# Kernel tuning notes

Measured on AMD Instinct MI355X. Metric: run time of the kernel, lower is better.

## Reference

```python
import jax, jax.numpy as jnp
import numpy as np

B, N, DIN, DH = 16, 512, 128, 256
NEG = -9.0e15  # matches -9000000000000000.0 in torch source


def _xavier(key, fan_in, fan_out):
    lim = float(np.sqrt(6.0 / (fan_in + fan_out)))
    return jax.random.uniform(key, (fan_in, fan_out), jnp.float32, -lim, lim)


def _l2n(x, eps=1e-12):
    # torch F.normalize: x / max(||x||, eps)
    return x / jnp.maximum(jnp.linalg.norm(x, axis=-1, keepdims=True), eps)


def _prelu(x, a):
    return jnp.where(x >= 0, x, a * x)


def setup_inputs() -> dict:
    key = jax.random.key(0)
    ks = jax.random.split(key, 12)
    seq = jax.random.normal(ks[0], (B, N, DIN), jnp.float32)
    # sparse-ish nonnegative adjacency with self loops, row-normalized
    u = jax.random.uniform(ks[1], (B, N, N), jnp.float32)
    a = jnp.where(u < 0.1, u, 0.0) + jnp.eye(N, dtype=jnp.float32)[None]
    adj = a / a.sum(-1, keepdims=True)
    # dense diffusion matrix, row-normalized
    d = jax.random.uniform(ks[2], (B, N, N), jnp.float32)
    diff = d / d.sum(-1, keepdims=True)
    # dropout keep-mask for F.dropout(p=0.1, training=True)
    keep = jax.random.bernoulli(ks[3], 0.9, (B, N, N)).astype(jnp.float32)
    drop_mask = keep / 0.9
    return {
        "seq": seq, "adj": adj, "diff": diff, "drop_mask": drop_mask,
        "fc1_w": _xavier(ks[4], DIN, DH),
        "q_w": _xavier(ks[5], DH, DH),
        "k_w": _xavier(ks[6], DH, DH),
        "v_w1": _xavier(ks[7], DH, DH),
        "v_w2": _xavier(ks[8], DH, DH),
        "fc2_w": _xavier(ks[9], DIN, DH),
        "bias1": jnp.zeros((DH,), jnp.float32),
        "bias2": jnp.zeros((DH,), jnp.float32),
        "prelu1_a": jnp.float32(0.25),
        "prelu2_a": jnp.float32(0.25),
        "v_prelu_a": jnp.float32(0.25),
    }


def reference(seq, adj, diff, drop_mask, fc1_w, q_w, k_w, v_w1, v_w2,
              fc2_w, bias1, bias2, prelu1_a, prelu2_a, v_prelu_a):
    # ---- GCN1 (attention branch) ----
    fts = seq @ fc1_w                                   # [B,N,H]
    out = jnp.einsum('bmn,bnh->bmh', adj, fts)          # adj aggregation
    q = _l2n(out @ q_w)
    k = _l2n(out @ k_w)
    scores = jax.lax.stop_gradient(jnp.einsum('bmd,bnd->bmn', q, k))  # .detach()
    div_loss = jnp.mean(jnp.sum((q - k) ** 2, axis=-1))
    att = jnp.where(adj > 0, scores, NEG)
    att = jax.nn.softmax(att, axis=-1) * drop_mask      # dropout(p=0.1)
    agg = jnp.einsum('bmn,bnh->bmh', att, out)
    v = _prelu(agg @ v_w1, v_prelu_a) @ v_w2 + bias1
    h1 = _prelu(v, prelu1_a)
    # ---- GCN2 (plain branch) ----
    h2 = _prelu(jnp.einsum('bmn,bnh->bmh', diff, seq @ fc2_w) + bias2, prelu2_a)
    # ---- Readout ----
    c1 = jnp.mean(h1, axis=1)                           # [B,H]
    c2 = jnp.mean(h2, axis=1)
    # ---- DIS ----
    n1 = _l2n(h1).reshape(B * N, DH)
    n2 = _l2n(h2).reshape(B * N, DH)
    node_logits = n1 @ n2.T                             # [B*N, B*N]
    graph_logits = _l2n(c1) @ _l2n(c2).T                # [B, B]
    return node_logits, graph_logits, div_loss
```

## Files before the change

### kernel.cpp

```cpp
#include <hip/hip_runtime.h>
#include <hip/hip_bf16.h>


using bf16x8 = __attribute__((ext_vector_type(8))) short;
using f32x4  = __attribute__((ext_vector_type(4))) float;

__device__ __forceinline__ unsigned short f2b(float f) {
    union { float f; unsigned int u; } x; x.f = f;
    unsigned int r = x.u + 0x7FFFu + ((x.u >> 16) & 1u);
    return (unsigned short)(r >> 16);
}
__device__ __forceinline__ void gload_lds16(const void* g, void* l) {
    __builtin_amdgcn_global_load_lds(
        (const __attribute__((address_space(1))) void*)g,
        (__attribute__((address_space(3))) void*)l, 16, 0, 0);
}

__global__ __launch_bounds__(256) void prep(
    const float* __restrict__ seq, const float* __restrict__ adj,
    const float* __restrict__ diff,
    const float* __restrict__ fc1, const float* __restrict__ fc2,
    const float* __restrict__ qw,  const float* __restrict__ kw,
    const float* __restrict__ v1,  const float* __restrict__ v2,
    unsigned short* __restrict__ seq_bf, unsigned short* __restrict__ adj_bf,
    unsigned short* __restrict__ diff_bf,
    unsigned short* fc1T, unsigned short* fc2T, unsigned short* qwT,
    unsigned short* kwT,  unsigned short* v1T,  unsigned short* v2T)
{
    __shared__ float t[32][33];
    const int bid = blockIdx.x, tid = threadIdx.x;
    if (bid < 9216) {
        long i = (long)bid * 256 + tid;
        const float* src; unsigned short* dst; long off;
        if (i < 262144)       { src = seq;  dst = seq_bf;  off = i; }
        else if (i < 1310720) { src = adj;  dst = adj_bf;  off = i - 262144; }
        else                  { src = diff; dst = diff_bf; off = i - 1310720; }
        float4 v = reinterpret_cast<const float4*>(src)[off];
        ushort4 o; o.x = f2b(v.x); o.y = f2b(v.y); o.z = f2b(v.z); o.w = f2b(v.w);
        reinterpret_cast<ushort4*>(dst)[off] = o;
        return;
    }
    const int r = bid - 9216;
    const int z = r >> 6;
    const float* in; unsigned short* op; int R;
    if      (z == 0) { in = fc1; op = fc1T; R = 128; }
    else if (z == 1) { in = fc2; op = fc2T; R = 128; }
    else if (z == 2) { in = qw;  op = qwT;  R = 256; }
    else if (z == 3) { in = kw;  op = kwT;  R = 256; }
    else if (z == 4) { in = v1;  op = v1T;  R = 256; }
    else             { in = v2;  op = v2T;  R = 256; }
    const int c0 = (r & 7) * 32, r0 = ((r >> 3) & 7) * 32;
    if (r0 >= R) return;
    const int x = tid & 31, y = tid >> 5;
    for (int i = 0; i < 32; i += 8) t[y + i][x] = in[(long)(r0 + y + i) * 256 + c0 + x];
    __syncthreads();
    for (int i = 0; i < 32; i += 8)
        op[(long)(c0 + y + i) * R + r0 + x] = f2b(t[x][y + i]);
}

#define BN 128
#define BK 64

template<int TBM, bool WF, bool WB, bool SWZ>
__global__ __launch_bounds__(256) void gemm_nt(
    const unsigned short* __restrict__ A, const unsigned short* __restrict__ Bt,
    float* __restrict__ Cf, unsigned short* __restrict__ Cb,
    int M, int Nn, int K, int lda, int ldb, int ldc,
    long sA, long sB, long sC)
{
    constexpr int MI = TBM / 32;
    __shared__ unsigned char smem_g[(TBM + BN) * BK * 2];
    unsigned short* As = (unsigned short*)smem_g;
    unsigned short* Bs = (unsigned short*)(smem_g + TBM * BK * 2);
    const int b = blockIdx.z;
    A  += (long)b * sA;
    Bt += (long)b * sB;
    const long cbase = (long)b * sC;

    int tx, ty;
    if (SWZ) {
        int bid = blockIdx.y * gridDim.x + blockIdx.x;
        int nwg = gridDim.x * gridDim.y;
        int cpx = nwg >> 3;
        int s = (bid & 7) * cpx + (bid >> 3);
        tx = s % gridDim.x; ty = s / gridDim.x;
    } else { tx = blockIdx.x; ty = blockIdx.y; }
    const int tile_m = ty * TBM;
    const int tile_n = tx * BN;

    const int tid  = threadIdx.x;
    const int lane = tid & 63;
    const int wave = tid >> 6;
    const int wm = (wave >> 1) * (TBM / 2);
    const int wn = (wave & 1) << 6;
    const int lrow = lane >> 3;
    const int lcol = (lane & 7) << 3;

    f32x4 acc[MI][4] = {};

    for (int k0 = 0; k0 < K; k0 += BK) {
        #pragma unroll
        for (int i = 0; i < TBM / 32; ++i) {
            const int rb = (i * 4 + wave) * 8;
            gload_lds16(A + (long)(tile_m + rb + lrow) * lda + k0 + lcol, &As[rb * BK]);
        }
        #pragma unroll
        for (int i = 0; i < 4; ++i) {
            const int rb = (i * 4 + wave) * 8;
            gload_lds16(Bt + (long)(tile_n + rb + lrow) * ldb + k0 + lcol, &Bs[rb * BK]);
        }
        __syncthreads();
        #pragma unroll
        for (int ks = 0; ks < 2; ++ks) {
            const int kk = ks * 32 + ((lane >> 4) << 3);
            bf16x8 af[MI], bq[4];
            #pragma unroll
            for (int mi = 0; mi < MI; ++mi)
                af[mi] = *reinterpret_cast<const bf16x8*>(&As[(wm + (lane & 15) + mi * 16) * BK + kk]);
            #pragma unroll
            for (int ni = 0; ni < 4; ++ni)
                bq[ni] = *reinterpret_cast<const bf16x8*>(&Bs[(wn + (lane & 15) + ni * 16) * BK + kk]);
            #pragma unroll
            for (int mi = 0; mi < MI; ++mi)
                #pragma unroll
                for (int ni = 0; ni < 4; ++ni)
                    acc[mi][ni] = __builtin_amdgcn_mfma_f32_16x16x32_bf16(
                        af[mi], bq[ni], acc[mi][ni], 0, 0, 0);
        }
        __syncthreads();
    }

    const int c0 = lane & 15;
    const int r0 = (lane >> 4) << 2;

    if (WB) {
        #pragma unroll
        for (int ni = 0; ni < 4; ++ni) {
            const int col = tile_n + wn + ni * 16 + c0;
            #pragma unroll
            for (int mi = 0; mi < MI; ++mi) {
                const int row0 = tile_m + wm + mi * 16 + r0;
                #pragma unroll
                for (int j = 0; j < 4; ++j)
                    Cb[cbase + (long)(row0 + j) * ldc + col] = f2b(acc[mi][ni][j]);
            }
        }
    }
    if (WF) {
        float* bounce = (float*)smem_g;
        const int tr = tid >> 5;
        const int tc = (tid & 31) << 2;
        #pragma unroll
        for (int h = 0; h < 2; ++h) {
            __syncthreads();
            if ((wave >> 1) == h) {
                #pragma unroll
                for (int mi = 0; mi < MI; ++mi)
                    #pragma unroll
                    for (int ni = 0; ni < 4; ++ni)
                        #pragma unroll
                        for (int j = 0; j < 4; ++j)
                            bounce[(mi * 16 + r0 + j) * 128 + wn + ni * 16 + c0] =
                                acc[mi][ni][j];
            }
            __syncthreads();
            #pragma unroll
            for (int p = 0; p < 8; ++p) {
                const int rl = p * 8 + tr;
                f32x4 v = *reinterpret_cast<const f32x4*>(&bounce[rl * 128 + tc]);
                __builtin_nontemporal_store(v, reinterpret_cast<f32x4*>(
                    &Cf[cbase + (long)(tile_m + h * 64 + rl) * ldc + tile_n + tc]));
            }
        }
    }
}

__global__ __launch_bounds__(256) void gcn1qk(
    const unsigned short* __restrict__ adj_bf,
    const unsigned short* __restrict__ ftsT,
    const unsigned short* __restrict__ qkT,
    unsigned short* __restrict__ outT,
    unsigned short* __restrict__ q_bf,
    unsigned short* __restrict__ k_bf)
{
    __shared__ unsigned char smem[73984];
    unsigned short* Ot  = (unsigned short*)smem;
    unsigned short* As  = (unsigned short*)(smem + 8448);
    unsigned short* Bs  = (unsigned short*)(smem + 10496);
    unsigned short* Bs2 = (unsigned short*)(smem + 8448);
    __shared__ float sred[16][4];

    const int b  = blockIdx.y;
    const int m0 = blockIdx.x << 4;
    const unsigned short* ap = adj_bf + ((long)b * 512 + m0) * 512;

    const int tid = threadIdx.x, lane = tid & 63, wave = tid >> 6;
    const int lrow = lane >> 3, lcol = (lane & 7) << 3;
    const int hi = lane >> 4, c0 = lane & 15, r0 = hi << 2;

    {
        const int wn = wave << 6;
        f32x4 acc[4] = {};
        for (int k0 = 0; k0 < 512; k0 += 64) {
            if (wave < 2)
                gload_lds16(ap + (long)(wave * 8 + lrow) * 512 + k0 + lcol, &As[wave * 8 * 64]);
            #pragma unroll
            for (int i = 0; i < 8; ++i) {
                const int rb = (i * 4 + wave) * 8;
                gload_lds16(ftsT + (long)(rb + lrow) * 8192 + b * 512 + k0 + lcol, &Bs[rb * 64]);
            }
            __syncthreads();
            #pragma unroll
            for (int ks = 0; ks < 2; ++ks) {
                const int kk = ks * 32 + (hi << 3);
                bf16x8 af = *reinterpret_cast<const bf16x8*>(&As[c0 * 64 + kk]);
                #pragma unroll
                for (int ni = 0; ni < 4; ++ni) {
                    bf16x8 bq = *reinterpret_cast<const bf16x8*>(&Bs[(wn + ni * 16 + c0) * 64 + kk]);
                    acc[ni] = __builtin_amdgcn_mfma_f32_16x16x32_bf16(af, bq, acc[ni], 0, 0, 0);
                }
            }
            __syncthreads();
        }
        #pragma unroll
        for (int ni = 0; ni < 4; ++ni) {
            const int col = wn + ni * 16 + c0;
            ushort4 o;
            unsigned short* e = (unsigned short*)&o;
            #pragma unroll
            for (int j = 0; j < 4; ++j) {
                unsigned short v = f2b(acc[ni][j]);
                e[j] = v;
                Ot[(r0 + j) * 264 + col] = v;
            }
            *reinterpret_cast<ushort4*>(
                &outT[(long)b * 131072 + (long)col * 512 + m0 + r0]) = o;
        }
    }

    {
        const int wn = wave << 7;
        f32x4 acc[8] = {};
        for (int k0 = 0; k0 < 256; k0 += 64) {
            #pragma unroll
            for (int i = 0; i < 16; ++i) {
                const int rb = (i * 4 + wave) * 8;
                gload_lds16(qkT + (long)(rb + lrow) * 256 + k0 + lcol, &Bs2[rb * 64]);
            }
            __syncthreads();
            #pragma unroll
            for (int ks = 0; ks < 2; ++ks) {
                const int kk = ks * 32 + (hi << 3);
                bf16x8 af = *reinterpret_cast<const bf16x8*>(&Ot[c0 * 264 + k0 + kk]);
                #pragma unroll
                for (int ni = 0; ni < 8; ++ni) {
                    bf16x8 bq = *reinterpret_cast<const bf16x8*>(&Bs2[(wn + ni * 16 + c0) * 64 + kk]);
                    acc[ni] = __builtin_amdgcn_mfma_f32_16x16x32_bf16(af, bq, acc[ni], 0, 0, 0);
                }
            }
            __syncthreads();
        }
        float rs[4] = {};
        #pragma unroll
        for (int ni = 0; ni < 8; ++ni)
            #pragma unroll
            for (int j = 0; j < 4; ++j) { float x = acc[ni][j]; rs[j] += x * x; }
        #pragma unroll
        for (int o = 1; o <= 8; o <<= 1)
            #pragma unroll
            for (int j = 0; j < 4; ++j) rs[j] += __shfl_xor(rs[j], o);
        if (c0 == 0) {
            #pragma unroll
            for (int j = 0; j < 4; ++j) sred[r0 + j][wave] = rs[j];
        }
        __syncthreads();
        float inv[4];
        #pragma unroll
        for (int j = 0; j < 4; ++j) {
            const int rr = r0 + j;
            float sq = sred[rr][0] + sred[rr][1];
            float sk = sred[rr][2] + sred[rr][3];
            inv[j] = 1.f / fmaxf(sqrtf(wave < 2 ? sq : sk), 1e-12f);
        }
        #pragma unroll
        for (int ni = 0; ni < 8; ++ni)
            #pragma unroll
            for (int j = 0; j < 4; ++j) {
                const long rowg = (long)b * 512 + m0 + r0 + j;
                const int col = wn + ni * 16 + c0;
                unsigned short v = f2b(acc[ni][j] * inv[j]);
                if (wave < 2) q_bf[rowg * 256 + col] = v;
                else          k_bf[rowg * 256 + col - 256] = v;
            }
    }
}

__global__ __launch_bounds__(256) void attmlp_h2(
    const unsigned short* __restrict__ q_bf,
    const unsigned short* __restrict__ k_bf,
    const unsigned short* __restrict__ adj_bf,
    const float* __restrict__ drop,
    const unsigned short* __restrict__ outT,
    const unsigned short* __restrict__ w1T,
    const unsigned short* __restrict__ w2T,
    const float* __restrict__ bias1,
    const float* __restrict__ av, const float* __restrict__ a1,
    unsigned short* __restrict__ n1,
    float* __restrict__ psum1,
    float* __restrict__ rowpart,
    const unsigned short* __restrict__ diff_bf,
    const unsigned short* __restrict__ fts2T,
    const float* __restrict__ bias2, const float* __restrict__ a2,
    unsigned short* __restrict__ n2,
    float* __restrict__ psum2)
{
    __shared__ unsigned char smem[69632];
    __shared__ float redm[32][4], reds[32][4];

    const int idx = blockIdx.x >> 1;
    const int tid = threadIdx.x, lane = tid & 63, wave = tid >> 6;
    const int lrow = lane >> 3, lcol = (lane & 7) << 3;
    const int hi = lane >> 4, c0 = lane & 15, r0 = hi << 2;

    if (blockIdx.x & 1) {
        unsigned short* As  = (unsigned short*)smem;
        unsigned short* Bs  = (unsigned short*)(smem + 4096);
        unsigned short* Pls = (unsigned short*)smem;
        unsigned short* Bs2 = (unsigned short*)(smem + 34816);
        unsigned short* T   = (unsigned short*)smem;
        unsigned short* Bs3 = (unsigned short*)(smem + 16896);

        const int b  = idx >> 4;
        const int m0 = (idx & 15) << 5;
        const unsigned short* qp = q_bf + (long)b * 131072 + (long)m0 * 256;
        const unsigned short* kp = k_bf + (long)b * 131072;
        const unsigned short* ot = outT + (long)b * 131072;
        const unsigned short* ap = adj_bf + ((long)b * 512 + m0) * 512;
        const float*          dp = drop   + ((long)b * 512 + m0) * 512;

        {
            const int wn = wave << 7;
            f32x4 acc[2][8] = {};
            for (int k0 = 0; k0 < 256; k0 += 64) {
                gload_lds16(qp + (long)(wave * 8 + lrow) * 256 + k0 + lcol, &As[wave * 8 * 64]);
                #pragma unroll
                for (int i = 0; i < 16; ++i) {
                    const int rb = (i * 4 + wave) * 8;
                    gload_lds16(kp + (long)(rb + lrow) * 256 + k0 + lcol, &Bs[rb * 64]);
                }
                __syncthreads();
                #pragma unroll
                for (int ks = 0; ks < 2; ++ks) {
                    const int kk = ks * 32 + (hi << 3);
                    bf16x8 af[2], bq[8];
                    #pragma unroll
                    for (int mi = 0; mi < 2; ++mi)
                        af[mi] = *reinterpret_cast<const bf16x8*>(&As[(mi * 16 + c0) * 64 + kk]);
                    #pragma unroll
                    for (int ni = 0; ni < 8; ++ni)
                        bq[ni] = *reinterpret_cast<const bf16x8*>(&Bs[(wn + ni * 16 + c0) * 64 + kk]);
                    #pragma unroll
                    for (int mi = 0; mi < 2; ++mi)
                        #pragma unroll
                        for (int ni = 0; ni < 8; ++ni)
                            acc[mi][ni] = __builtin_amdgcn_mfma_f32_16x16x32_bf16(
                                af[mi], bq[ni], acc[mi][ni], 0, 0, 0);
                }
                __syncthreads();
            }

            float rmax[2][4];
            #pragma unroll
            for (int mi = 0; mi < 2; ++mi)
                #pragma unroll
                for (int j = 0; j < 4; ++j) rmax[mi][j] = -3.0e38f;
            #pragma unroll
            for (int mi = 0; mi < 2; ++mi)
                #pragma unroll
                for (int ni = 0; ni < 8; ++ni)
                    #pragma unroll
                    for (int j = 0; j < 4; ++j) {
                        const int rowl = mi * 16 + r0 + j;
                        const int col  = wn + ni * 16 + c0;
                        float s = acc[mi][ni][j];
                        if (col == m0 + rowl)
                            rowpart[(long)b * 512 + m0 + rowl] = 2.f - 2.f * s;
                        bool m = ap[(long)rowl * 512 + col] != 0;
                        s = m ? s : -3.0e38f;
                        acc[mi][ni][j] = s;
                        rmax[mi][j] = fmaxf(rmax[mi][j], s);
                    }
            #pragma unroll
            for (int o = 1; o <= 8; o <<= 1)
                #pragma unroll
                for (int mi = 0; mi < 2; ++mi)
                    #pragma unroll
                    for (int j = 0; j < 4; ++j)
                        rmax[mi][j] = fmaxf(rmax[mi][j], __shfl_xor(rmax[mi][j], o));
            if (c0 == 0) {
                #pragma unroll
                for (int mi = 0; mi < 2; ++mi)
                    #pragma unroll
                    for (int j = 0; j < 4; ++j) redm[mi * 16 + r0 + j][wave] = rmax[mi][j];
            }
            __syncthreads();
            float mx[2][4], rsum[2][4];
            #pragma unroll
            for (int mi = 0; mi < 2; ++mi)
                #pragma unroll
                for (int j = 0; j < 4; ++j) {
                    const int rr = mi * 16 + r0 + j;
                    mx[mi][j] = fmaxf(fmaxf(redm[rr][0], redm[rr][1]),
                                      fmaxf(redm[rr][2], redm[rr][3]));
                    rsum[mi][j] = 0.f;
                }
            #pragma unroll
            for (int mi = 0; mi < 2; ++mi)
                #pragma unroll
                for (int ni = 0; ni < 8; ++ni)
                    #pragma unroll
                    for (int j = 0; j < 4; ++j) {
                        float e = __expf(acc[mi][ni][j] - mx[mi][j]);
                        acc[mi][ni][j] = e;
                        rsum[mi][j] += e;
                    }
            #pragma unroll
            for (int o = 1; o <= 8; o <<= 1)
                #pragma unroll
                for (int mi = 0; mi < 2; ++mi)
                    #pragma unroll
                    for (int j = 0; j < 4; ++j) rsum[mi][j] += __shfl_xor(rsum[mi][j], o);
            if (c0 == 0) {
                #pragma unroll
                for (int mi = 0; mi < 2; ++mi)
                    #pragma unroll
                    for (int j = 0; j < 4; ++j) reds[mi * 16 + r0 + j][wave] = rsum[mi][j];
            }
            __syncthreads();
            float inv[2][4];
            #pragma unroll
            for (int mi = 0; mi < 2; ++mi)
                #pragma unroll
                for (int j = 0; j < 4; ++j) {
                    const int rr = mi * 16 + r0 + j;
                    inv[mi][j] = 1.f / (reds[rr][0] + reds[rr][1] + reds[rr][2] + reds[rr][3]);
                }
            #pragma unroll
            for (int mi = 0; mi < 2; ++mi)
                #pragma unroll
                for (int ni = 0; ni < 8; ++ni)
                    #pragma unroll
                    for (int j = 0; j < 4; ++j) {
                        const int rowl = mi * 16 + r0 + j;
                        const int col  = wn + ni * 16 + c0;
                        float p = acc[mi][ni][j] * inv[mi][j] * dp[(long)rowl * 512 + col];
                        Pls[rowl * 520 + col] = f2b(p);
                    }
        }
        __syncthreads();

        f32x4 acc2[2][4] = {};
        {
            const int wn = wave << 6;
            for (int k0 = 0; k0 < 512; k0 += 64) {
                #pragma unroll
                for (int i = 0; i < 8; ++i) {
                    const int rb = (i * 4 + wave) * 8;
                    gload_lds16(ot + (long)(rb + lrow) * 512 + k0 + lcol, &Bs2[rb * 64]);
                }
                __syncthreads();
                #pragma unroll
                for (int ks = 0; ks < 2; ++ks) {
                    const int kk = ks * 32 + (hi << 3);
                    bf16x8 af[2], bq[4];
                    #pragma unroll
                    for (int mi = 0; mi < 2; ++mi)
                        af[mi] = *reinterpret_cast<const bf16x8*>(&Pls[(mi * 16 + c0) * 520 + k0 + kk]);
                    #pragma unroll
                    for (int ni = 0; ni < 4; ++ni)
                        bq[ni] = *reinterpret_cast<const bf16x8*>(&Bs2[(wn + ni * 16 + c0) * 64 + kk]);
                    #pragma unroll
                    for (int mi = 0; mi < 2; ++mi)
                        #pragma unroll
                        for (int ni = 0; ni < 4; ++ni)
                            acc2[mi][ni] = __builtin_amdgcn_mfma_f32_16x16x32_bf16(
                                af[mi], bq[ni], acc2[mi][ni], 0, 0, 0);
                }
                __syncthreads();
            }
        }

        const int wn6 = wave << 6;
        const float alphav = av[0];
        #pragma unroll
        for (int mi = 0; mi < 2; ++mi)
            #pragma unroll
            for (int ni = 0; ni < 4; ++ni)
                #pragma unroll
                for (int j = 0; j < 4; ++j)
                    T[(mi * 16 + r0 + j) * 264 + wn6 + ni * 16 + c0] = f2b(acc2[mi][ni][j]);
        f32x4 acct[2][4] = {};
        for (int k0 = 0; k0 < 256; k0 += 64) {
            #pragma unroll
            for (int i = 0; i < 8; ++i) {
                const int rb = (i * 4 + wave) * 8;
                gload_lds16(w1T + (long)(rb + lrow) * 256 + k0 + lcol, &Bs3[rb * 64]);
            }
            __syncthreads();
            #pragma unroll
            for (int ks = 0; ks < 2; ++ks) {
                const int kk = ks * 32 + (hi << 3);
                bf16x8 af[2], bq[4];
                #pragma unroll
                for (int mi = 0; mi < 2; ++mi)
                    af[mi] = *reinterpret_cast<const bf16x8*>(&T[(mi * 16 + c0) * 264 + k0 + kk]);
                #pragma unroll
                for (int ni = 0; ni < 4; ++ni)
                    bq[ni] = *reinterpret_cast<const bf16x8*>(&Bs3[(wn6 + ni * 16 + c0) * 64 + kk]);
                #pragma unroll
                for (int mi = 0; mi < 2; ++mi)
                    #pragma unroll
                    for (int ni = 0; ni < 4; ++ni)
                        acct[mi][ni] = __builtin_amdgcn_mfma_f32_16x16x32_bf16(
                            af[mi], bq[ni], acct[mi][ni], 0, 0, 0);
            }
            __syncthreads();
        }
        #pragma unroll
        for (int mi = 0; mi < 2; ++mi)
            #pragma unroll
            for (int ni = 0; ni < 4; ++ni)
                #pragma unroll
                for (int j = 0; j < 4; ++j) {
                    float x = acct[mi][ni][j];
                    x = (x >= 0.f) ? x : alphav * x;
                    T[(mi * 16 + r0 + j) * 264 + wn6 + ni * 16 + c0] = f2b(x);
                }

        f32x4 acc3[2][4] = {};
        for (int k0 = 0; k0 < 256; k0 += 64) {
            #pragma unroll
            for (int i = 0; i < 8; ++i) {
                const int rb = (i * 4 + wave) * 8;
                gload_lds16(w2T + (long)(rb + lrow) * 256 + k0 + lcol, &Bs3[rb * 64]);
            }
            __syncthreads();
            #pragma unroll
            for (int ks = 0; ks < 2; ++ks) {
                const int kk = ks * 32 + (hi << 3);
                bf16x8 af[2], bq[4];
                #pragma unroll
                for (int mi = 0; mi < 2; ++mi)
                    af[mi] = *reinterpret_cast<const bf16x8*>(&T[(mi * 16 + c0) * 264 + k0 + kk]);
                #pragma unroll
                for (int ni = 0; ni < 4; ++ni)
                    bq[ni] = *reinterpret_cast<const bf16x8*>(&Bs3[(wn6 + ni * 16 + c0) * 64 + kk]);
                #pragma unroll
                for (int mi = 0; mi < 2; ++mi)
                    #pragma unroll
                    for (int ni = 0; ni < 4; ++ni)
                        acc3[mi][ni] = __builtin_amdgcn_mfma_f32_16x16x32_bf16(
                            af[mi], bq[ni], acc3[mi][ni], 0, 0, 0);
            }
            __syncthreads();
        }

        const float alpha1 = a1[0];
        float rs[2][4] = {};
        #pragma unroll
        for (int ni = 0; ni < 4; ++ni) {
            const float bv = bias1[wn6 + ni * 16 + c0];
            #pragma unroll
            for (int mi = 0; mi < 2; ++mi)
                #pragma unroll
                for (int j = 0; j < 4; ++j) {
                    float x = acc3[mi][ni][j] + bv;
                    x = (x >= 0.f) ? x : alpha1 * x;
                    acc3[mi][ni][j] = x;
                    rs[mi][j] += x * x;
                }
        }
        #pragma unroll
        for (int o = 1; o <= 8; o <<= 1)
            #pragma unroll
            for (int mi = 0; mi < 2; ++mi)
                #pragma unroll
                for (int j = 0; j < 4; ++j) rs[mi][j] += __shfl_xor(rs[mi][j], o);
        if (c0 == 0) {
            #pragma unroll
            for (int mi = 0; mi < 2; ++mi)
                #pragma unroll
                for (int j = 0; j < 4; ++j) redm[mi * 16 + r0 + j][wave] = rs[mi][j];
        }
        __syncthreads();
        float inv2[2][4];
        #pragma unroll
        for (int mi = 0; mi < 2; ++mi)
            #pragma unroll
            for (int j = 0; j < 4; ++j) {
                const int rr = mi * 16 + r0 + j;
                float s = redm[rr][0] + redm[rr][1] + redm[rr][2] + redm[rr][3];
                inv2[mi][j] = 1.f / fmaxf(sqrtf(s), 1e-12f);
            }
        float cs[4];
        #pragma unroll
        for (int ni = 0; ni < 4; ++ni) {
            float s = 0.f;
            #pragma unroll
            for (int mi = 0; mi < 2; ++mi)
                #pragma unroll
                for (int j = 0; j < 4; ++j) s += acc3[mi][ni][j];
            s += __shfl_xor(s, 16);
            s += __shfl_xor(s, 32);
            cs[ni] = s;
        }
        if (lane < 16) {
            #pragma unroll
            for (int ni = 0; ni < 4; ++ni)
                psum1[(long)idx * 256 + wn6 + ni * 16 + lane] = cs[ni];
        }
        const long row0g = (long)b * 512 + m0;
        #pragma unroll
        for (int mi = 0; mi < 2; ++mi)
            #pragma unroll
            for (int ni = 0; ni < 4; ++ni)
                #pragma unroll
                for (int j = 0; j < 4; ++j)
                    n1[(row0g + mi * 16 + r0 + j) * 256 + wn6 + ni * 16 + c0] =
                        f2b(acc3[mi][ni][j] * inv2[mi][j]);
    } else {
        unsigned short* As = (unsigned short*)smem;
        unsigned short* Bs = (unsigned short*)(smem + 4096);

        const int z = idx >> 4;
        const int arow0 = (idx & 15) << 5;
        const unsigned short* A = diff_bf + (long)z * 262144;
        const unsigned short* Bt = fts2T + z * 512;
        const int wn = wave << 6;

        f32x4 acc[2][4] = {};
        for (int k0 = 0; k0 < 512; k0 += 64) {
            {
                const int rb = wave * 8;
                gload_lds16(A + (long)(arow0 + rb + lrow) * 512 + k0 + lcol, &As[rb * 64]);
            }
            #pragma unroll
            for (int i = 0; i < 8; ++i) {
                const int rb = (i * 4 + wave) * 8;
                gload_lds16(Bt + (long)(rb + lrow) * 8192 + k0 + lcol, &Bs[rb * 64]);
            }
            __syncthreads();
            #pragma unroll
            for (int ks = 0; ks < 2; ++ks) {
                const int kk = ks * 32 + (hi << 3);
                bf16x8 af[2], bq[4];
                #pragma unroll
                for (int mi = 0; mi < 2; ++mi)
                    af[mi] = *reinterpret_cast<const bf16x8*>(&As[(mi * 16 + c0) * 64 + kk]);
                #pragma unroll
                for (int ni = 0; ni < 4; ++ni)
                    bq[ni] = *reinterpret_cast<const bf16x8*>(&Bs[(wn + ni * 16 + c0) * 64 + kk]);
                #pragma unroll
                for (int mi = 0; mi < 2; ++mi)
                    #pragma unroll
                    for (int ni = 0; ni < 4; ++ni)
                        acc[mi][ni] = __builtin_amdgcn_mfma_f32_16x16x32_bf16(
                            af[mi], bq[ni], acc[mi][ni], 0, 0, 0);
            }
            __syncthreads();
        }

        const float alpha = a2[0];
        float rs[2][4] = {};
        #pragma unroll
        for (int ni = 0; ni < 4; ++ni) {
            const float bv = bias2[wn + ni * 16 + c0];
            #pragma unroll
            for (int mi = 0; mi < 2; ++mi)
                #pragma unroll
                for (int j = 0; j < 4; ++j) {
                    float x = acc[mi][ni][j] + bv;
                    x = (x >= 0.f) ? x : alpha * x;
                    acc[mi][ni][j] = x;
                    rs[mi][j] += x * x;
                }
        }
        #pragma unroll
        for (int o = 1; o <= 8; o <<= 1)
            #pragma unroll
            for (int mi = 0; mi < 2; ++mi)
                #pragma unroll
                for (int j = 0; j < 4; ++j) rs[mi][j] += __shfl_xor(rs[mi][j], o);
        if (c0 == 0) {
            #pragma unroll
            for (int mi = 0; mi < 2; ++mi)
                #pragma unroll
                for (int j = 0; j < 4; ++j) redm[mi * 16 + r0 + j][wave] = rs[mi][j];
        }
        __syncthreads();
        float inv[2][4];
        #pragma unroll
        for (int mi = 0; mi < 2; ++mi)
            #pragma unroll
            for (int j = 0; j < 4; ++j) {
                const int rr = mi * 16 + r0 + j;
                float s = redm[rr][0] + redm[rr][1] + redm[rr][2] + redm[rr][3];
                inv[mi][j] = 1.f / fmaxf(sqrtf(s), 1e-12f);
            }
        float cs[4];
        #pragma unroll
        for (int ni = 0; ni < 4; ++ni) {
            float s = 0.f;
            #pragma unroll
            for (int mi = 0; mi < 2; ++mi)
                #pragma unroll
                for (int j = 0; j < 4; ++j) s += acc[mi][ni][j];
            s += __shfl_xor(s, 16);
            s += __shfl_xor(s, 32);
            cs[ni] = s;
        }
        if (lane < 16) {
            #pragma unroll
            for (int ni = 0; ni < 4; ++ni)
                psum2[(long)idx * 256 + wn + ni * 16 + lane] = cs[ni];
        }
        const long grow0 = (long)idx * 32;
        #pragma unroll
        for (int mi = 0; mi < 2; ++mi)
            #pragma unroll
            for (int ni = 0; ni < 4; ++ni)
                #pragma unroll
                for (int j = 0; j < 4; ++j)
                    n2[(grow0 + mi * 16 + r0 + j) * 256 + wn + ni * 16 + c0] =
                        f2b(acc[mi][ni][j] * inv[mi][j]);
    }
}

__global__ __launch_bounds__(256) void readout(
    const float* __restrict__ psum1, const float* __restrict__ psum2,
    const float* __restrict__ rowpart,
    float* __restrict__ out_g, float* __restrict__ out_div)
{
    __shared__ float c1s[16][256], c2s[16][256];
    __shared__ float invn[32];
    const int t = threadIdx.x;
    for (int g = 0; g < 16; ++g) {
        float s1 = 0.f, s2 = 0.f;
        #pragma unroll
        for (int c = 0; c < 16; ++c) {
            s1 += psum1[(long)(g * 16 + c) * 256 + t];
            s2 += psum2[(long)(g * 16 + c) * 256 + t];
        }
        c1s[g][t] = s1 * (1.f / 512.f);
        c2s[g][t] = s2 * (1.f / 512.f);
    }
    __syncthreads();
    if (t < 32) {
        const float* row = (t < 16) ? c1s[t] : c2s[t - 16];
        float ss = 0.f;
        for (int h = 0; h < 256; ++h) { float v = row[h]; ss += v * v; }
        invn[t] = 1.f / fmaxf(sqrtf(ss), 1e-12f);
    }
    __syncthreads();
    const int ii = t >> 4, jj = t & 15;
    float s = 0.f;
    for (int h = 0; h < 256; ++h) s += c1s[ii][h] * c2s[jj][h];
    out_g[ii * 16 + jj] = s * invn[ii] * invn[16 + jj];
    float ds = 0.f;
    for (int i = t; i < 8192; i += 256) ds += rowpart[i];
    #pragma unroll
    for (int o = 32; o; o >>= 1) ds += __shfl_xor(ds, o);
    __shared__ float red[4];
    if ((t & 63) == 0) red[t >> 6] = ds;
    __syncthreads();
    if (t == 0) out_div[0] = (red[0] + red[1] + red[2] + red[3]) * (1.f / 8192.f);
}

static constexpr long OFF_SEQ_BF  = 0;
static constexpr long OFF_FC1T    = 2097152;
static constexpr long OFF_QWT     = 2228224;
static constexpr long OFF_VW1T    = 2490368;
static constexpr long OFF_VW2T    = 2621440;
static constexpr long OFF_ADJ     = 3145728;
static constexpr long OFF_DIFF    = 11534336;
static constexpr long OFF_FTST    = 19922944;
static constexpr long OFF_OUTT    = 28311552;
static constexpr long OFF_QBF     = 32505856;
static constexpr long OFF_KBF     = 36700160;
static constexpr long OFF_N1      = 40894464;
static constexpr long OFF_N2      = 45088768;
static constexpr long OFF_PSUM    = 49283072;
static constexpr long OFF_ROWPART = 49807360;

extern "C" void kernel_launch(void* const* d_in, const int* in_sizes, int n_in,
                              void* d_out, int out_size, void* d_ws, size_t ws_size,
                              hipStream_t stream) {
    const float* seq      = (const float*)d_in[0];
    const float* adj      = (const float*)d_in[1];
    const float* diff     = (const float*)d_in[2];
    const float* drop     = (const float*)d_in[3];
    const float* fc1_w    = (const float*)d_in[4];
    const float* q_w      = (const float*)d_in[5];
    const float* k_w      = (const float*)d_in[6];
    const float* v_w1     = (const float*)d_in[7];
    const float* v_w2     = (const float*)d_in[8];
    const float* fc2_w    = (const float*)d_in[9];
    const float* bias1    = (const float*)d_in[10];
    const float* bias2    = (const float*)d_in[11];
    const float* prelu1_a = (const float*)d_in[12];
    const float* prelu2_a = (const float*)d_in[13];
    const float* v_prelu  = (const float*)d_in[14];
    float* out = (float*)d_out;

    char* ws = (char*)d_ws;
    unsigned short* seq_bf  = (unsigned short*)(ws + OFF_SEQ_BF);
    unsigned short* fc1T    = (unsigned short*)(ws + OFF_FC1T);
    unsigned short* fc2T    = (unsigned short*)(ws + OFF_FC1T + 65536);
    unsigned short* qwT     = (unsigned short*)(ws + OFF_QWT);
    unsigned short* kwT     = (unsigned short*)(ws + OFF_QWT + 131072);
    unsigned short* vw1T    = (unsigned short*)(ws + OFF_VW1T);
    unsigned short* vw2T    = (unsigned short*)(ws + OFF_VW2T);
    unsigned short* adj_bf  = (unsigned short*)(ws + OFF_ADJ);
    unsigned short* diff_bf = (unsigned short*)(ws + OFF_DIFF);
    unsigned short* ftsT    = (unsigned short*)(ws + OFF_FTST);
    unsigned short* fts2T   = (unsigned short*)(ws + OFF_FTST + 4194304);
    unsigned short* outT    = (unsigned short*)(ws + OFF_OUTT);
    unsigned short* q_bf    = (unsigned short*)(ws + OFF_QBF);
    unsigned short* k_bf    = (unsigned short*)(ws + OFF_KBF);
    unsigned short* n1_bf   = (unsigned short*)(ws + OFF_N1);
    unsigned short* n2_bf   = (unsigned short*)(ws + OFF_N2);
    float*          psum1   = (float*)(ws + OFF_PSUM);
    float*          psum2   = (float*)(ws + OFF_PSUM + 262144);
    float*          rowpart = (float*)(ws + OFF_ROWPART);

    prep<<<9600, 256, 0, stream>>>(seq, adj, diff, fc1_w, fc2_w, q_w, k_w, v_w1, v_w2,
                                   seq_bf, adj_bf, diff_bf, fc1T, fc2T, qwT, kwT, vw1T, vw2T);

    gemm_nt<64, false, true, false><<<dim3(64, 4, 2), 256, 0, stream>>>(
        fc1T, seq_bf, nullptr, ftsT,
        256, 8192, 128, 128, 128, 8192, 32768, 0, 2097152);

    gcn1qk<<<dim3(32, 16), 256, 0, stream>>>(adj_bf, ftsT, qwT, outT, q_bf, k_bf);

    attmlp_h2<<<512, 256, 0, stream>>>(
        q_bf, k_bf, adj_bf, drop, outT, vw1T, vw2T, bias1, v_prelu, prelu1_a,
        n1_bf, psum1, rowpart,
        diff_bf, fts2T, bias2, prelu2_a, n2_bf, psum2);

    readout<<<1, 256, 0, stream>>>(psum1, psum2, rowpart, out + 67108864, out + 67109120);

    gemm_nt<128, true, false, true><<<dim3(64, 64, 1), 256, 0, stream>>>(
        n1_bf, n2_bf, out, nullptr,
        8192, 8192, 256, 256, 256, 8192, 0, 0, 0);

    (void)in_sizes; (void)n_in; (void)out_size; (void)ws_size;
}
```

Measured before the change: 206.1 us.

## Load MFMA fragments directly from global memory and fuse readout into final GEMM

In gcn1qk and attmlp_h2, the LDS-staged GEMM loops (global_load_lds plus barriers) are replaced with direct per-lane 16-byte global loads feeding the MFMA instructions. This drops most LDS traffic and block barriers and cuts shared memory use, which may allow more resident blocks. The cost is uncoalesced, redundant global/L2 reads. The separate one-block readout kernel is removed and its work moved into block (0,0) of the final node-logits GEMM, saving one launch.

```diff
diff --git a/kernel.cpp b/kernel.cpp
--- a/kernel.cpp
+++ b/kernel.cpp
@@ -14,6 +14,9 @@
     __builtin_amdgcn_global_load_lds(
         (const __attribute__((address_space(1))) void*)g,
         (__attribute__((address_space(3))) void*)l, 16, 0, 0);
+}
+__device__ __forceinline__ bf16x8 ldfrag(const unsigned short* p) {
+    return *reinterpret_cast<const bf16x8*>(p);
 }
 
 __global__ __launch_bounds__(256) void prep(
@@ -61,15 +64,20 @@
 #define BN 128
 #define BK 64
 
-template<int TBM, bool WF, bool WB, bool SWZ>
+template<int TBM, bool WF, bool WB, bool SWZ, bool RD>
 __global__ __launch_bounds__(256) void gemm_nt(
     const unsigned short* __restrict__ A, const unsigned short* __restrict__ Bt,
     float* __restrict__ Cf, unsigned short* __restrict__ Cb,
     int M, int Nn, int K, int lda, int ldb, int ldc,
-    long sA, long sB, long sC)
+    long sA, long sB, long sC,
+    const float* __restrict__ rd_psum1, const float* __restrict__ rd_psum2,
+    const float* __restrict__ rd_rowpart,
+    float* __restrict__ rd_outg, float* __restrict__ rd_outdiv)
 {
     constexpr int MI = TBM / 32;
     __shared__ unsigned char smem_g[(TBM + BN) * BK * 2];
+    __shared__ float rd_invn[32];
+    __shared__ float rd_red[4];
     unsigned short* As = (unsigned short*)smem_g;
     unsigned short* Bs = (unsigned short*)(smem_g + TBM * BK * 2);
     const int b = blockIdx.z;
@@ -116,10 +124,10 @@
             bf16x8 af[MI], bq[4];
             #pragma unroll
             for (int mi = 0; mi < MI; ++mi)
-                af[mi] = *reinterpret_cast<const bf16x8*>(&As[(wm + (lane & 15) + mi * 16) * BK + kk]);
+                af[mi] = ldfrag(&As[(wm + (lane & 15) + mi * 16) * BK + kk]);
             #pragma unroll
             for (int ni = 0; ni < 4; ++ni)
-                bq[ni] = *reinterpret_cast<const bf16x8*>(&Bs[(wn + (lane & 15) + ni * 16) * BK + kk]);
+                bq[ni] = ldfrag(&Bs[(wn + (lane & 15) + ni * 16) * BK + kk]);
             #pragma unroll
             for (int mi = 0; mi < MI; ++mi)
                 #pragma unroll
@@ -171,6 +179,44 @@
                 __builtin_nontemporal_store(v, reinterpret_cast<f32x4*>(
                     &Cf[cbase + (long)(tile_m + h * 64 + rl) * ldc + tile_n + tc]));
             }
+        }
+    }
+    if (RD) {
+        if (blockIdx.x == 0 && blockIdx.y == 0) {
+            __syncthreads();
+            float* c1s = (float*)smem_g;
+            float* c2s = c1s + 4096;
+            const int t = tid;
+            for (int g = 0; g < 16; ++g) {
+                float s1 = 0.f, s2 = 0.f;
+                #pragma unroll
+                for (int c = 0; c < 16; ++c) {
+                    s1 += rd_psum1[(long)(g * 16 + c) * 256 + t];
+                    s2 += rd_psum2[(long)(g * 16 + c) * 256 + t];
+                }
+                c1s[g * 256 + t] = s1 * (1.f / 512.f);
+                c2s[g * 256 + t] = s2 * (1.f / 512.f);
+            }
+            __syncthreads();
+            if (t < 32) {
+                const float* row = (t < 16) ? &c1s[t * 256] : &c2s[(t - 16) * 256];
+                float ss = 0.f;
+                for (int h = 0; h < 256; ++h) { float v = row[h]; ss += v * v; }
+                rd_invn[t] = 1.f / fmaxf(sqrtf(ss), 1e-12f);
+            }
+            __syncthreads();
+            const int ii = t >> 4, jj = t & 15;
+            float s = 0.f;
+            for (int h = 0; h < 256; ++h) s += c1s[ii * 256 + h] * c2s[jj * 256 + h];
+            rd_outg[ii * 16 + jj] = s * rd_invn[ii] * rd_invn[16 + jj];
+            float ds = 0.f;
+            for (int i = t; i < 8192; i += 256) ds += rd_rowpart[i];
+            #pragma unroll
+            for (int o = 32; o; o >>= 1) ds += __shfl_xor(ds, o);
+            if ((t & 63) == 0) rd_red[t >> 6] = ds;
+            __syncthreads();
+            if (t == 0)
+                rd_outdiv[0] = (rd_red[0] + rd_red[1] + rd_red[2] + rd_red[3]) * (1.f / 8192.f);
         }
     }
 }
@@ -183,44 +229,27 @@
     unsigned short* __restrict__ q_bf,
     unsigned short* __restrict__ k_bf)
 {
-    __shared__ unsigned char smem[73984];
-    unsigned short* Ot  = (unsigned short*)smem;
-    unsigned short* As  = (unsigned short*)(smem + 8448);
-    unsigned short* Bs  = (unsigned short*)(smem + 10496);
-    unsigned short* Bs2 = (unsigned short*)(smem + 8448);
+    __shared__ unsigned short Ot[16 * 264];
     __shared__ float sred[16][4];
 
     const int b  = blockIdx.y;
     const int m0 = blockIdx.x << 4;
-    const unsigned short* ap = adj_bf + ((long)b * 512 + m0) * 512;
-
     const int tid = threadIdx.x, lane = tid & 63, wave = tid >> 6;
-    const int lrow = lane >> 3, lcol = (lane & 7) << 3;
     const int hi = lane >> 4, c0 = lane & 15, r0 = hi << 2;
+    const int ko = hi << 3;
 
     {
         const int wn = wave << 6;
+        const unsigned short* ap = adj_bf + ((long)b * 512 + m0 + c0) * 512;
         f32x4 acc[4] = {};
-        for (int k0 = 0; k0 < 512; k0 += 64) {
-            if (wave < 2)
-                gload_lds16(ap + (long)(wave * 8 + lrow) * 512 + k0 + lcol, &As[wave * 8 * 64]);
-            #pragma unroll
-            for (int i = 0; i < 8; ++i) {
-                const int rb = (i * 4 + wave) * 8;
-                gload_lds16(ftsT + (long)(rb + lrow) * 8192 + b * 512 + k0 + lcol, &Bs[rb * 64]);
-            }
-            __syncthreads();
-            #pragma unroll
-            for (int ks = 0; ks < 2; ++ks) {
-                const int kk = ks * 32 + (hi << 3);
-                bf16x8 af = *reinterpret_cast<const bf16x8*>(&As[c0 * 64 + kk]);
-                #pragma unroll
-                for (int ni = 0; ni < 4; ++ni) {
-                    bf16x8 bq = *reinterpret_cast<const bf16x8*>(&Bs[(wn + ni * 16 + c0) * 64 + kk]);
-                    acc[ni] = __builtin_amdgcn_mfma_f32_16x16x32_bf16(af, bq, acc[ni], 0, 0, 0);
-                }
-            }
-            __syncthreads();
+        #pragma unroll 2
+        for (int k0 = 0; k0 < 512; k0 += 32) {
+            bf16x8 af = ldfrag(ap + k0 + ko);
+            #pragma unroll
+            for (int ni = 0; ni < 4; ++ni) {
+                bf16x8 bq = ldfrag(ftsT + (long)(wn + ni * 16 + c0) * 8192 + b * 512 + k0 + ko);
+                acc[ni] = __builtin_amdgcn_mfma_f32_16x16x32_bf16(af, bq, acc[ni], 0, 0, 0);
+            }
         }
         #pragma unroll
         for (int ni = 0; ni < 4; ++ni) {
@@ -237,28 +266,19 @@
                 &outT[(long)b * 131072 + (long)col * 512 + m0 + r0]) = o;
         }
     }
+    __syncthreads();
 
     {
         const int wn = wave << 7;
         f32x4 acc[8] = {};
-        for (int k0 = 0; k0 < 256; k0 += 64) {
-            #pragma unroll
-            for (int i = 0; i < 16; ++i) {
-                const int rb = (i * 4 + wave) * 8;
-                gload_lds16(qkT + (long)(rb + lrow) * 256 + k0 + lcol, &Bs2[rb * 64]);
-            }
-            __syncthreads();
-            #pragma unroll
-            for (int ks = 0; ks < 2; ++ks) {
-                const int kk = ks * 32 + (hi << 3);
-                bf16x8 af = *reinterpret_cast<const bf16x8*>(&Ot[c0 * 264 + k0 + kk]);
-                #pragma unroll
-                for (int ni = 0; ni < 8; ++ni) {
-                    bf16x8 bq = *reinterpret_cast<const bf16x8*>(&Bs2[(wn + ni * 16 + c0) * 64 + kk]);
-                    acc[ni] = __builtin_amdgcn_mfma_f32_16x16x32_bf16(af, bq, acc[ni], 0, 0, 0);
-                }
-            }
-            __syncthreads();
+        #pragma unroll 2
+        for (int k0 = 0; k0 < 256; k0 += 32) {
+            bf16x8 af = ldfrag(&Ot[c0 * 264 + k0 + ko]);
+            #pragma unroll
+            for (int ni = 0; ni < 8; ++ni) {
+                bf16x8 bq = ldfrag(qkT + (long)(wn + ni * 16 + c0) * 256 + k0 + ko);
+                acc[ni] = __builtin_amdgcn_mfma_f32_16x16x32_bf16(af, bq, acc[ni], 0, 0, 0);
+            }
         }
         float rs[4] = {};
         #pragma unroll
@@ -314,25 +334,21 @@
     unsigned short* __restrict__ n2,
     float* __restrict__ psum2)
 {
-    __shared__ unsigned char smem[69632];
+    __shared__ unsigned char smem[33280];
     __shared__ float redm[32][4], reds[32][4];
 
     const int idx = blockIdx.x >> 1;
     const int tid = threadIdx.x, lane = tid & 63, wave = tid >> 6;
-    const int lrow = lane >> 3, lcol = (lane & 7) << 3;
     const int hi = lane >> 4, c0 = lane & 15, r0 = hi << 2;
+    const int ko = hi << 3;
 
     if (blockIdx.x & 1) {
-        unsigned short* As  = (unsigned short*)smem;
-        unsigned short* Bs  = (unsigned short*)(smem + 4096);
         unsigned short* Pls = (unsigned short*)smem;
-        unsigned short* Bs2 = (unsigned short*)(smem + 34816);
         unsigned short* T   = (unsigned short*)smem;
-        unsigned short* Bs3 = (unsigned short*)(smem + 16896);
 
         const int b  = idx >> 4;
         const int m0 = (idx & 15) << 5;
-        const unsigned short* qp = q_bf + (long)b * 131072 + (long)m0 * 256;
+        const unsigned short* qp = q_bf + (long)b * 131072;
         const unsigned short* kp = k_bf + (long)b * 131072;
         const unsigned short* ot = outT + (long)b * 131072;
         const unsigned short* ap = adj_bf + ((long)b * 512 + m0) * 512;
@@ -341,32 +357,20 @@
         {
             const int wn = wave << 7;
             f32x4 acc[2][8] = {};
-            for (int k0 = 0; k0 < 256; k0 += 64) {
-                gload_lds16(qp + (long)(wave * 8 + lrow) * 256 + k0 + lcol, &As[wave * 8 * 64]);
-                #pragma unroll
-                for (int i = 0; i < 16; ++i) {
-                    const int rb = (i * 4 + wave) * 8;
-                    gload_lds16(kp + (long)(rb + lrow) * 256 + k0 + lcol, &Bs[rb * 64]);
+            #pragma unroll 2
+            for (int k0 = 0; k0 < 256; k0 += 32) {
+                bf16x8 af[2];
+                #pragma unroll
+                for (int mi = 0; mi < 2; ++mi)
+                    af[mi] = ldfrag(qp + (long)(m0 + mi * 16 + c0) * 256 + k0 + ko);
+                #pragma unroll
+                for (int ni = 0; ni < 8; ++ni) {
+                    bf16x8 bq = ldfrag(kp + (long)(wn + ni * 16 + c0) * 256 + k0 + ko);
+                    #pragma unroll
+                    for (int mi = 0; mi < 2; ++mi)
+                        acc[mi][ni] = __builtin_amdgcn_mfma_f32_16x16x32_bf16(
+                            af[mi], bq, acc[mi][ni], 0, 0, 0);
                 }
-                __syncthreads();
-                #pragma unroll
-                for (int ks = 0; ks < 2; ++ks) {
-                    const int kk = ks * 32 + (hi << 3);
-                    bf16x8 af[2], bq[8];
-                    #pragma unroll
-                    for (int mi = 0; mi < 2; ++mi)
-                        af[mi] = *reinterpret_cast<const bf16x8*>(&As[(mi * 16 + c0) * 64 + kk]);
-                    #pragma unroll
-                    for (int ni = 0; ni < 8; ++ni)
-                        bq[ni] = *reinterpret_cast<const bf16x8*>(&Bs[(wn + ni * 16 + c0) * 64 + kk]);
-                    #pragma unroll
-                    for (int mi = 0; mi < 2; ++mi)
-                        #pragma unroll
-                        for (int ni = 0; ni < 8; ++ni)
-                            acc[mi][ni] = __builtin_amdgcn_mfma_f32_16x16x32_bf16(
-                                af[mi], bq[ni], acc[mi][ni], 0, 0, 0);
-                }
-                __syncthreads();
             }
 
             float rmax[2][4];
@@ -462,33 +466,23 @@
         f32x4 acc2[2][4] = {};
         {
             const int wn = wave << 6;
-            for (int k0 = 0; k0 < 512; k0 += 64) {
-                #pragma unroll
-                for (int i = 0; i < 8; ++i) {
-                    const int rb = (i * 4 + wave) * 8;
-                    gload_lds16(ot + (long)(rb + lrow) * 512 + k0 + lcol, &Bs2[rb * 64]);
+            #pragma unroll 2
+            for (int k0 = 0; k0 < 512; k0 += 32) {
+                bf16x8 af[2];
+                #pragma unroll
+                for (int mi = 0; mi < 2; ++mi)
+                    af[mi] = ldfrag(&Pls[(mi * 16 + c0) * 520 + k0 + ko]);
+                #pragma unroll
+                for (int ni = 0; ni < 4; ++ni) {
+                    bf16x8 bq = ldfrag(ot + (long)(wn + ni * 16 + c0) * 512 + k0 + ko);
+                    #pragma unroll
+                    for (int mi = 0; mi < 2; ++mi)
+                        acc2[mi][ni] = __builtin_amdgcn_mfma_f32_16x16x32_bf16(
+                            af[mi], bq, acc2[mi][ni], 0, 0, 0);
                 }
-                __syncthreads();
-                #pragma unroll
-                for (int ks = 0; ks < 2; ++ks) {
-                    const int kk = ks * 32 + (hi << 3);
-                    bf16x8 af[2], bq[4];
-                    #pragma unroll
-                    for (int mi = 0; mi < 2; ++mi)
-                        af[mi] = *reinterpret_cast<const bf16x8*>(&Pls[(mi * 16 + c0) * 520 + k0 + kk]);
-                    #pragma unroll
-                    for (int ni = 0; ni < 4; ++ni)
-                        bq[ni] = *reinterpret_cast<const bf16x8*>(&Bs2[(wn + ni * 16 + c0) * 64 + kk]);
-                    #pragma unroll
-                    for (int mi = 0; mi < 2; ++mi)
-                        #pragma unroll
-                        for (int ni = 0; ni < 4; ++ni)
-                            acc2[mi][ni] = __builtin_amdgcn_mfma_f32_16x16x32_bf16(
-                                af[mi], bq[ni], acc2[mi][ni], 0, 0, 0);
-                }
-                __syncthreads();
-            }
-        }
+            }
+        }
+        __syncthreads();
 
         const int wn6 = wave << 6;
         const float alphav = av[0];
@@ -499,33 +493,24 @@
                 #pragma unroll
                 for (int j = 0; j < 4; ++j)
                     T[(mi * 16 + r0 + j) * 264 + wn6 + ni * 16 + c0] = f2b(acc2[mi][ni][j]);
+        __syncthreads();
         f32x4 acct[2][4] = {};
-        for (int k0 = 0; k0 < 256; k0 += 64) {
-            #pragma unroll
-            for (int i = 0; i < 8; ++i) {
-                const int rb = (i * 4 + wave) * 8;
-                gload_lds16(w1T + (long)(rb + lrow) * 256 + k0 + lcol, &Bs3[rb * 64]);
-            }
-            __syncthreads();
-            #pragma unroll
-            for (int ks = 0; ks < 2; ++ks) {
-                const int kk = ks * 32 + (hi << 3);
-                bf16x8 af[2], bq[4];
-                #pragma unroll
-                for (int mi = 0; mi < 2; ++mi)
-                    af[mi] = *reinterpret_cast<const bf16x8*>(&T[(mi * 16 + c0) * 264 + k0 + kk]);
-                #pragma unroll
-                for (int ni = 0; ni < 4; ++ni)
-                    bq[ni] = *reinterpret_cast<const bf16x8*>(&Bs3[(wn6 + ni * 16 + c0) * 64 + kk]);
-                #pragma unroll
-                for (int mi = 0; mi < 2; ++mi)
-                    #pragma unroll
-                    for (int ni = 0; ni < 4; ++ni)
-                        acct[mi][ni] = __builtin_amdgcn_mfma_f32_16x16x32_bf16(
-                            af[mi], bq[ni], acct[mi][ni], 0, 0, 0);
-            }
-            __syncthreads();
-        }
+        #pragma unroll 2
+        for (int k0 = 0; k0 < 256; k0 += 32) {
+            bf16x8 af[2];
+            #pragma unroll
+            for (int mi = 0; mi < 2; ++mi)
+                af[mi] = ldfrag(&T[(mi * 16 + c0) * 264 + k0 + ko]);
+            #pragma unroll
+            for (int ni = 0; ni < 4; ++ni) {
+                bf16x8 bq = ldfrag(w1T + (long)(wn6 + ni * 16 + c0) * 256 + k0 + ko);
+                #pragma unroll
+                for (int mi = 0; mi < 2; ++mi)
+                    acct[mi][ni] = __builtin_amdgcn_mfma_f32_16x16x32_bf16(
+                        af[mi], bq, acct[mi][ni], 0, 0, 0);
+            }
+        }
+        __syncthreads();
         #pragma unroll
         for (int mi = 0; mi < 2; ++mi)
             #pragma unroll
@@ -536,33 +521,23 @@
                     x = (x >= 0.f) ? x : alphav * x;
                     T[(mi * 16 + r0 + j) * 264 + wn6 + ni * 16 + c0] = f2b(x);
                 }
+        __syncthreads();
 
         f32x4 acc3[2][4] = {};
-        for (int k0 = 0; k0 < 256; k0 += 64) {
-            #pragma unroll
-            for (int i = 0; i < 8; ++i) {
-                const int rb = (i * 4 + wave) * 8;
-                gload_lds16(w2T + (long)(rb + lrow) * 256 + k0 + lcol, &Bs3[rb * 64]);
-            }
-            __syncthreads();
-            #pragma unroll
-            for (int ks = 0; ks < 2; ++ks) {
-                const int kk = ks * 32 + (hi << 3);
-                bf16x8 af[2], bq[4];
-                #pragma unroll
-                for (int mi = 0; mi < 2; ++mi)
-                    af[mi] = *reinterpret_cast<const bf16x8*>(&T[(mi * 16 + c0) * 264 + k0 + kk]);
-                #pragma unroll
-                for (int ni = 0; ni < 4; ++ni)
-                    bq[ni] = *reinterpret_cast<const bf16x8*>(&Bs3[(wn6 + ni * 16 + c0) * 64 + kk]);
-                #pragma unroll
-                for (int mi = 0; mi < 2; ++mi)
-                    #pragma unroll
-                    for (int ni = 0; ni < 4; ++ni)
-                        acc3[mi][ni] = __builtin_amdgcn_mfma_f32_16x16x32_bf16(
-                            af[mi], bq[ni], acc3[mi][ni], 0, 0, 0);
-            }
-            __syncthreads();
+        #pragma unroll 2
+        for (int k0 = 0; k0 < 256; k0 += 32) {
+            bf16x8 af[2];
+            #pragma unroll
+            for (int mi = 0; mi < 2; ++mi)
+                af[mi] = ldfrag(&T[(mi * 16 + c0) * 264 + k0 + ko]);
+            #pragma unroll
+            for (int ni = 0; ni < 4; ++ni) {
+                bf16x8 bq = ldfrag(w2T + (long)(wn6 + ni * 16 + c0) * 256 + k0 + ko);
+                #pragma unroll
+                for (int mi = 0; mi < 2; ++mi)
+                    acc3[mi][ni] = __builtin_amdgcn_mfma_f32_16x16x32_bf16(
+                        af[mi], bq, acc3[mi][ni], 0, 0, 0);
+            }
         }
 
         const float alpha1 = a1[0];
@@ -586,6 +561,7 @@
             for (int mi = 0; mi < 2; ++mi)
                 #pragma unroll
                 for (int j = 0; j < 4; ++j) rs[mi][j] += __shfl_xor(rs[mi][j], o);
+        __syncthreads();
         if (c0 == 0) {
             #pragma unroll
             for (int mi = 0; mi < 2; ++mi)
@@ -629,45 +605,27 @@
                     n1[(row0g + mi * 16 + r0 + j) * 256 + wn6 + ni * 16 + c0] =
                         f2b(acc3[mi][ni][j] * inv2[mi][j]);
     } else {
-        unsigned short* As = (unsigned short*)smem;
-        unsigned short* Bs = (unsigned short*)(smem + 4096);
-
         const int z = idx >> 4;
         const int arow0 = (idx & 15) << 5;
-        const unsigned short* A = diff_bf + (long)z * 262144;
-        const unsigned short* Bt = fts2T + z * 512;
+        const unsigned short* ad = diff_bf + (long)z * 262144;
+        const unsigned short* bt = fts2T + z * 512;
         const int wn = wave << 6;
 
         f32x4 acc[2][4] = {};
-        for (int k0 = 0; k0 < 512; k0 += 64) {
-            {
-                const int rb = wave * 8;
-                gload_lds16(A + (long)(arow0 + rb + lrow) * 512 + k0 + lcol, &As[rb * 64]);
-            }
-            #pragma unroll
-            for (int i = 0; i < 8; ++i) {
-                const int rb = (i * 4 + wave) * 8;
-                gload_lds16(Bt + (long)(rb + lrow) * 8192 + k0 + lcol, &Bs[rb * 64]);
-            }
-            __syncthreads();
-            #pragma unroll
-            for (int ks = 0; ks < 2; ++ks) {
-                const int kk = ks * 32 + (hi << 3);
-                bf16x8 af[2], bq[4];
-                #pragma unroll
-                for (int mi = 0; mi < 2; ++mi)
-                    af[mi] = *reinterpret_cast<const bf16x8*>(&As[(mi * 16 + c0) * 64 + kk]);
-                #pragma unroll
-                for (int ni = 0; ni < 4; ++ni)
-                    bq[ni] = *reinterpret_cast<const bf16x8*>(&Bs[(wn + ni * 16 + c0) * 64 + kk]);
-                #pragma unroll
-                for (int mi = 0; mi < 2; ++mi)
-                    #pragma unroll
-                    for (int ni = 0; ni < 4; ++ni)
-                        acc[mi][ni] = __builtin_amdgcn_mfma_f32_16x16x32_bf16(
-                            af[mi], bq[ni], acc[mi][ni], 0, 0, 0);
-            }
-            __syncthreads();
+        #pragma unroll 2
+        for (int k0 = 0; k0 < 512; k0 += 32) {
+            bf16x8 af[2];
+            #pragma unroll
+            for (int mi = 0; mi < 2; ++mi)
+                af[mi] = ldfrag(ad + (long)(arow0 + mi * 16 + c0) * 512 + k0 + ko);
+            #pragma unroll
+            for (int ni = 0; ni < 4; ++ni) {
+                bf16x8 bq = ldfrag(bt + (long)(wn + ni * 16 + c0) * 8192 + k0 + ko);
+                #pragma unroll
+                for (int mi = 0; mi < 2; ++mi)
+                    acc[mi][ni] = __builtin_amdgcn_mfma_f32_16x16x32_bf16(
+                        af[mi], bq, acc[mi][ni], 0, 0, 0);
+            }
         }
 
         const float alpha = a2[0];
@@ -734,46 +692,6 @@
                     n2[(grow0 + mi * 16 + r0 + j) * 256 + wn + ni * 16 + c0] =
                         f2b(acc[mi][ni][j] * inv[mi][j]);
     }
-}
-
-__global__ __launch_bounds__(256) void readout(
-    const float* __restrict__ psum1, const float* __restrict__ psum2,
-    const float* __restrict__ rowpart,
-    float* __restrict__ out_g, float* __restrict__ out_div)
-{
-    __shared__ float c1s[16][256], c2s[16][256];
-    __shared__ float invn[32];
-    const int t = threadIdx.x;
-    for (int g = 0; g < 16; ++g) {
-        float s1 = 0.f, s2 = 0.f;
-        #pragma unroll
-        for (int c = 0; c < 16; ++c) {
-            s1 += psum1[(long)(g * 16 + c) * 256 + t];
-            s2 += psum2[(long)(g * 16 + c) * 256 + t];
-        }
-        c1s[g][t] = s1 * (1.f / 512.f);
-        c2s[g][t] = s2 * (1.f / 512.f);
-    }
-    __syncthreads();
-    if (t < 32) {
-        const float* row = (t < 16) ? c1s[t] : c2s[t - 16];
-        float ss = 0.f;
-        for (int h = 0; h < 256; ++h) { float v = row[h]; ss += v * v; }
-        invn[t] = 1.f / fmaxf(sqrtf(ss), 1e-12f);
-    }
-    __syncthreads();
-    const int ii = t >> 4, jj = t & 15;
-    float s = 0.f;
-    for (int h = 0; h < 256; ++h) s += c1s[ii][h] * c2s[jj][h];
-    out_g[ii * 16 + jj] = s * invn[ii] * invn[16 + jj];
-    float ds = 0.f;
-    for (int i = t; i < 8192; i += 256) ds += rowpart[i];
-    #pragma unroll
-    for (int o = 32; o; o >>= 1) ds += __shfl_xor(ds, o);
-    __shared__ float red[4];
-    if ((t & 63) == 0) red[t >> 6] = ds;
-    __syncthreads();
-    if (t == 0) out_div[0] = (red[0] + red[1] + red[2] + red[3]) * (1.f / 8192.f);
 }
 
 static constexpr long OFF_SEQ_BF  = 0;
@@ -836,9 +754,10 @@
     prep<<<9600, 256, 0, stream>>>(seq, adj, diff, fc1_w, fc2_w, q_w, k_w, v_w1, v_w2,
                                    seq_bf, adj_bf, diff_bf, fc1T, fc2T, qwT, kwT, vw1T, vw2T);
 
-    gemm_nt<64, false, true, false><<<dim3(64, 4, 2), 256, 0, stream>>>(
+    gemm_nt<64, false, true, false, false><<<dim3(64, 4, 2), 256, 0, stream>>>(
         fc1T, seq_bf, nullptr, ftsT,
-        256, 8192, 128, 128, 128, 8192, 32768, 0, 2097152);
+        256, 8192, 128, 128, 128, 8192, 32768, 0, 2097152,
+        nullptr, nullptr, nullptr, nullptr, nullptr);
 
     gcn1qk<<<dim3(32, 16), 256, 0, stream>>>(adj_bf, ftsT, qwT, outT, q_bf, k_bf);
 
@@ -847,11 +766,10 @@
         n1_bf, psum1, rowpart,
         diff_bf, fts2T, bias2, prelu2_a, n2_bf, psum2);
 
-    readout<<<1, 256, 0, stream>>>(psum1, psum2, rowpart, out + 67108864, out + 67109120);
-
-    gemm_nt<128, true, false, true><<<dim3(64, 64, 1), 256, 0, stream>>>(
+    gemm_nt<128, true, false, true, true><<<dim3(64, 64, 1), 256, 0, stream>>>(
         n1_bf, n2_bf, out, nullptr,
-        8192, 8192, 256, 256, 256, 8192, 0, 0, 0);
+        8192, 8192, 256, 256, 256, 8192, 0, 0, 0,
+        psum1, psum2, rowpart, out + 67108864, out + 67109120);
 
     (void)in_sizes; (void)n_in; (void)out_size; (void)ws_size;
 }
```

New measurement: 195.4 us (median of 2 runs). -5.2%, faster.
